# Kernel tuning notes

Measured on AMD Instinct MI355X. Metric: run time of the kernel, lower is better.

## Reference

```python
import jax, jax.numpy as jnp
import numpy as np

N_NODES = 100000
N_EDGES = 1250000
D_FEAT = 64


def setup_inputs() -> dict:
    key = jax.random.key(0)
    k1, k2, k3 = jax.random.split(key, 3)
    inputs = jax.random.normal(k1, (N_NODES, D_FEAT), dtype=jnp.float32)
    src = jax.random.randint(k2, (N_EDGES,), 0, N_NODES, dtype=jnp.int32)
    dst = jax.random.randint(k3, (N_EDGES,), 0, N_NODES, dtype=jnp.int32)
    return {"inputs": inputs, "src": src, "dst": dst}


def reference(inputs, src, dst):
    # copy_src: message on each edge is the source node's feature -> gather
    msgs = inputs[src]  # [E, d]
    # gcn_reduce: max over mailbox (incoming messages) per destination node
    agg = jax.ops.segment_max(msgs, dst, num_segments=N_NODES)  # [N, d], -inf for empty
    # Nodes receiving no messages keep their original feature (DGL recv semantics)
    indeg = jax.ops.segment_sum(jnp.ones((src.shape[0],), dtype=jnp.int32), dst,
                                num_segments=N_NODES)  # [N]
    v_feature = jnp.where((indeg > 0)[:, None], agg, inputs)  # [N, d]
    return jnp.concatenate([inputs, v_feature], axis=1)  # [N, 2d]
```

## Files before the change

### kernel.cpp

```cpp
#include <hip/hip_runtime.h>
#include <math.h>

#define D_FEAT 64
#define SCAN_BLOCK 1024


__global__ void zero_kernel(int* __restrict__ p, int n) {
    int i = blockIdx.x * blockDim.x + threadIdx.x;
    if (i < n) p[i] = 0;
}

__global__ void hist_kernel(const int* __restrict__ dst, int* __restrict__ counts,
                            int n_edges) {
    int stride = gridDim.x * blockDim.x;
    for (int e = blockIdx.x * blockDim.x + threadIdx.x; e < n_edges; e += stride) {
        atomicAdd(&counts[dst[e]], 1);
    }
}

__global__ void scanA_kernel(const int* __restrict__ counts,
                             int* __restrict__ offsets,
                             int* __restrict__ blocksums, int n) {
    __shared__ int smem[SCAN_BLOCK];
    int tid = threadIdx.x;
    int i = blockIdx.x * SCAN_BLOCK + tid;
    int v = (i < n) ? counts[i] : 0;
    smem[tid] = v;
    __syncthreads();
    for (int off = 1; off < SCAN_BLOCK; off <<= 1) {
        int t = (tid >= off) ? smem[tid - off] : 0;
        __syncthreads();
        smem[tid] += t;
        __syncthreads();
    }
    if (i < n) offsets[i] = smem[tid] - v;
    if (tid == SCAN_BLOCK - 1) blocksums[blockIdx.x] = smem[tid];
}

__global__ void scanB_kernel(int* __restrict__ blocksums, int nb) {
    __shared__ int smem[SCAN_BLOCK];
    int tid = threadIdx.x;
    int v = (tid < nb) ? blocksums[tid] : 0;
    smem[tid] = v;
    __syncthreads();
    for (int off = 1; off < SCAN_BLOCK; off <<= 1) {
        int t = (tid >= off) ? smem[tid - off] : 0;
        __syncthreads();
        smem[tid] += t;
        __syncthreads();
    }
    if (tid < nb) blocksums[tid] = smem[tid] - v;
}

__global__ void scanC_kernel(int* __restrict__ offsets, int* __restrict__ cursor,
                             const int* __restrict__ blocksums, int n, int n_edges) {
    int i = blockIdx.x * SCAN_BLOCK + threadIdx.x;
    if (i < n) {
        int o = offsets[i] + blocksums[blockIdx.x];
        offsets[i] = o;
        cursor[i] = o;
    }
    if (i == 0) offsets[n] = n_edges;
}

__global__ void scatter_kernel(const int* __restrict__ src,
                               const int* __restrict__ dst,
                               int* __restrict__ cursor,
                               int* __restrict__ sorted_src, int n_edges) {
    int stride = gridDim.x * blockDim.x;
    for (int e = blockIdx.x * blockDim.x + threadIdx.x; e < n_edges; e += stride) {
        int pos = atomicAdd(&cursor[dst[e]], 1);
        sorted_src[pos] = src[e];
    }
}

__global__ void pull_max_kernel(const float* __restrict__ inp,
                                const int* __restrict__ offsets,
                                const int* __restrict__ sorted_src,
                                float* __restrict__ out, int n_nodes) {
    int gtid = blockIdx.x * blockDim.x + threadIdx.x;
    int node = gtid >> 6;
    if (node >= n_nodes) return;
    int lane = threadIdx.x & 63;
    int g = lane >> 4;
    int l = lane & 15;

    int beg = offsets[node];
    int end = offsets[node + 1];

    const float4* inp4 = reinterpret_cast<const float4*>(inp);
    float4 own = inp4[(size_t)node * 16 + l];

    float4 m;
    m.x = -INFINITY; m.y = -INFINITY; m.z = -INFINITY; m.w = -INFINITY;
    for (int j = beg + g; j < end; j += 4) {
        int s = sorted_src[j];
        float4 v = inp4[(size_t)s * 16 + l];
        m.x = fmaxf(m.x, v.x);
        m.y = fmaxf(m.y, v.y);
        m.z = fmaxf(m.z, v.z);
        m.w = fmaxf(m.w, v.w);
    }
    m.x = fmaxf(m.x, __shfl_xor(m.x, 16, 64));
    m.y = fmaxf(m.y, __shfl_xor(m.y, 16, 64));
    m.z = fmaxf(m.z, __shfl_xor(m.z, 16, 64));
    m.w = fmaxf(m.w, __shfl_xor(m.w, 16, 64));
    m.x = fmaxf(m.x, __shfl_xor(m.x, 32, 64));
    m.y = fmaxf(m.y, __shfl_xor(m.y, 32, 64));
    m.z = fmaxf(m.z, __shfl_xor(m.z, 32, 64));
    m.w = fmaxf(m.w, __shfl_xor(m.w, 32, 64));

    if (beg == end) m = own;

    float4* out4 = reinterpret_cast<float4*>(out);
    if (lane < 16) {
        out4[(size_t)node * 32 + l] = own;
    } else if (lane < 32) {
        out4[(size_t)node * 32 + 16 + l] = m;
    }
}

extern "C" void kernel_launch(void* const* d_in, const int* in_sizes, int n_in,
                              void* d_out, int out_size, void* d_ws, size_t ws_size,
                              hipStream_t stream) {
    const float* inp = (const float*)d_in[0];
    const int* src = (const int*)d_in[1];
    const int* dst = (const int*)d_in[2];
    float* out = (float*)d_out;

    int n_nodes = in_sizes[0] / D_FEAT;
    int n_edges = in_sizes[1];

    int nScanBlocks = (n_nodes + SCAN_BLOCK - 1) / SCAN_BLOCK;

    int* ws = (int*)d_ws;
    int* counts_cursor = ws;
    int* offsets = ws + n_nodes;
    int* blocksums = ws + 2 * n_nodes + 1;
    int* sorted_src = ws + 2 * n_nodes + 1 + nScanBlocks;

    {
        int block = 256;
        int grid = (n_nodes + block - 1) / block;
        zero_kernel<<<grid, block, 0, stream>>>(counts_cursor, n_nodes);
    }
    hist_kernel<<<2048, 256, 0, stream>>>(dst, counts_cursor, n_edges);
    scanA_kernel<<<nScanBlocks, SCAN_BLOCK, 0, stream>>>(counts_cursor, offsets,
                                                         blocksums, n_nodes);
    scanB_kernel<<<1, SCAN_BLOCK, 0, stream>>>(blocksums, nScanBlocks);
    scanC_kernel<<<nScanBlocks, SCAN_BLOCK, 0, stream>>>(offsets, counts_cursor,
                                                         blocksums, n_nodes, n_edges);
    scatter_kernel<<<2048, 256, 0, stream>>>(src, dst, counts_cursor,
                                             sorted_src, n_edges);
    {
        int total = n_nodes * 64;
        int block = 256;
        int grid = (total + block - 1) / block;
        pull_max_kernel<<<grid, block, 0, stream>>>(inp, offsets, sorted_src,
                                                    out, n_nodes);
    }
}
```

Measured before the change: 300.5 us.

## Partition histogram and scatter atomics by destination node range across blocks

Histogram and scatter kernels now assign each block one of 8 destination-node ranges, and each block scans its edge chunk while only performing atomics for destinations in its range. The intent is to localize atomic traffic so that blocks with the same blockIdx mod 8 (likely mapped to the same XCD) hit a smaller node subset, improving L2 locality of atomics on the multi-die MI355X. The cost is that every edge's dst is read 8 times and src reads are filtered, which adds redundant global loads.

```diff
diff --git a/kernel.cpp b/kernel.cpp
--- a/kernel.cpp
+++ b/kernel.cpp
@@ -3,6 +3,7 @@
 
 #define D_FEAT 64
 #define SCAN_BLOCK 1024
+#define N_RANGES 8
 
 
 __global__ void zero_kernel(int* __restrict__ p, int n) {
@@ -10,11 +11,18 @@
     if (i < n) p[i] = 0;
 }
 
-__global__ void hist_kernel(const int* __restrict__ dst, int* __restrict__ counts,
-                            int n_edges) {
-    int stride = gridDim.x * blockDim.x;
-    for (int e = blockIdx.x * blockDim.x + threadIdx.x; e < n_edges; e += stride) {
-        atomicAdd(&counts[dst[e]], 1);
+__global__ void hist_part_kernel(const int* __restrict__ dst,
+                                 int* __restrict__ counts,
+                                 int n_edges, int nodes_per_range) {
+    int r = blockIdx.x & (N_RANGES - 1);
+    int c = blockIdx.x / N_RANGES;
+    int nchunks = gridDim.x / N_RANGES;
+    int lo = r * nodes_per_range;
+    int hi = lo + nodes_per_range;
+    int stride = nchunks * blockDim.x;
+    for (int e = c * blockDim.x + threadIdx.x; e < n_edges; e += stride) {
+        int d = dst[e];
+        if (d >= lo && d < hi) atomicAdd(&counts[d], 1);
     }
 }
 
@@ -63,14 +71,23 @@
     if (i == 0) offsets[n] = n_edges;
 }
 
-__global__ void scatter_kernel(const int* __restrict__ src,
-                               const int* __restrict__ dst,
-                               int* __restrict__ cursor,
-                               int* __restrict__ sorted_src, int n_edges) {
-    int stride = gridDim.x * blockDim.x;
-    for (int e = blockIdx.x * blockDim.x + threadIdx.x; e < n_edges; e += stride) {
-        int pos = atomicAdd(&cursor[dst[e]], 1);
-        sorted_src[pos] = src[e];
+__global__ void scatter_part_kernel(const int* __restrict__ src,
+                                    const int* __restrict__ dst,
+                                    int* __restrict__ cursor,
+                                    int* __restrict__ sorted_src,
+                                    int n_edges, int nodes_per_range) {
+    int r = blockIdx.x & (N_RANGES - 1);
+    int c = blockIdx.x / N_RANGES;
+    int nchunks = gridDim.x / N_RANGES;
+    int lo = r * nodes_per_range;
+    int hi = lo + nodes_per_range;
+    int stride = nchunks * blockDim.x;
+    for (int e = c * blockDim.x + threadIdx.x; e < n_edges; e += stride) {
+        int d = dst[e];
+        if (d >= lo && d < hi) {
+            int pos = atomicAdd(&cursor[d], 1);
+            sorted_src[pos] = src[e];
+        }
     }
 }
 
@@ -132,6 +149,7 @@
     int n_edges = in_sizes[1];
 
     int nScanBlocks = (n_nodes + SCAN_BLOCK - 1) / SCAN_BLOCK;
+    int nodes_per_range = (n_nodes + N_RANGES - 1) / N_RANGES;
 
     int* ws = (int*)d_ws;
     int* counts_cursor = ws;
@@ -144,14 +162,16 @@
         int grid = (n_nodes + block - 1) / block;
         zero_kernel<<<grid, block, 0, stream>>>(counts_cursor, n_nodes);
     }
-    hist_kernel<<<2048, 256, 0, stream>>>(dst, counts_cursor, n_edges);
+    hist_part_kernel<<<N_RANGES * 160, 256, 0, stream>>>(dst, counts_cursor,
+                                                         n_edges, nodes_per_range);
     scanA_kernel<<<nScanBlocks, SCAN_BLOCK, 0, stream>>>(counts_cursor, offsets,
                                                          blocksums, n_nodes);
     scanB_kernel<<<1, SCAN_BLOCK, 0, stream>>>(blocksums, nScanBlocks);
     scanC_kernel<<<nScanBlocks, SCAN_BLOCK, 0, stream>>>(offsets, counts_cursor,
                                                          blocksums, n_nodes, n_edges);
-    scatter_kernel<<<2048, 256, 0, stream>>>(src, dst, counts_cursor,
-                                             sorted_src, n_edges);
+    scatter_part_kernel<<<N_RANGES * 160, 256, 0, stream>>>(src, dst, counts_cursor,
+                                                            sorted_src, n_edges,
+                                                            nodes_per_range);
     {
         int total = n_nodes * 64;
         int block = 256;
```

Result: faster. 256.7 us (-14.6%).
